# Optimization experiments

Measured on AMD Instinct MI355X. Metric: run time of the kernel, lower is better.

Reference implementation:

```python
import jax, jax.numpy as jnp
import numpy as np

HIDDEN = 1024
HEADS = 16
HEAD_DIM = HIDDEN // HEADS  # 64
MLP_HIDDEN = int(HIDDEN * 4.0)  # 4096
B, L = 2, 2048
EPS_LN = 1e-6
EPS_RMS = 1e-6


def setup_inputs() -> dict:
    key = jax.random.key(0)
    ks = jax.random.split(key, 12)
    s = 0.02
    return {
        "x": jax.random.normal(ks[0], (B, L, HIDDEN), jnp.float32),
        "vec": jax.random.normal(ks[1], (B, HIDDEN), jnp.float32),
        "pe": jax.random.normal(ks[2], (1, 1, L, HEAD_DIM // 2, 2, 2), jnp.float32),
        "w_mod": jax.random.normal(ks[3], (HIDDEN, 3 * HIDDEN), jnp.float32) * s,
        "b_mod": jnp.zeros((3 * HIDDEN,), jnp.float32),
        "w1": jax.random.normal(ks[4], (HIDDEN, 3 * HIDDEN + MLP_HIDDEN), jnp.float32) * s,
        "b1": jnp.zeros((3 * HIDDEN + MLP_HIDDEN,), jnp.float32),
        "w_mlp": jax.random.normal(ks[5], (MLP_HIDDEN, HIDDEN), jnp.float32) * s,
        "b_mlp": jnp.zeros((HIDDEN,), jnp.float32),
        "w2": jax.random.normal(ks[6], (2 * HIDDEN, HIDDEN), jnp.float32) * s,
        "b2": jnp.zeros((HIDDEN,), jnp.float32),
        "q_scale": jnp.ones((HEAD_DIM,), jnp.float32),
        "k_scale": jnp.ones((HEAD_DIM,), jnp.float32),
    }


def _layernorm(x, eps=EPS_LN):
    m = jnp.mean(x, axis=-1, keepdims=True)
    v = jnp.mean(jnp.square(x - m), axis=-1, keepdims=True)
    return (x - m) * jax.lax.rsqrt(v + eps)


def _rmsnorm(x, scale, eps=EPS_RMS):
    rrms = jax.lax.rsqrt(jnp.mean(jnp.square(x), axis=-1, keepdims=True) + eps)
    return x * rrms * scale


def _apply_rope(t, pe):
    # t: [B,H,L,D]; pe: [1,1,L,D//2,2,2]
    t_ = t.reshape(*t.shape[:-1], -1, 1, 2)  # [B,H,L,D//2,1,2]
    out = pe[..., 0] * t_[..., 0] + pe[..., 1] * t_[..., 1]  # [B,H,L,D//2,2]
    return out.reshape(t.shape)


def reference(x, vec, pe, w_mod, b_mod, w1, b1, w_mlp, b_mlp, w2, b2, q_scale, k_scale):
    # adaLN modulation: silu(vec) -> Dense(3*dim) -> shift, scale, gate
    mod = (jax.nn.silu(vec) @ w_mod + b_mod)[:, None, :]  # [B,1,3H]
    shift, scale, gate = jnp.split(mod, 3, axis=-1)
    x_mod = (1.0 + scale) * _layernorm(x) + shift
    # fused QKV + MLP projection
    h = x_mod @ w1 + b1  # [B,L,3H+MH]
    qkv, mlp = h[..., : 3 * HIDDEN], h[..., 3 * HIDDEN :]
    qkv = qkv.reshape(x.shape[0], x.shape[1], 3, HEADS, HEAD_DIM)
    qkv = jnp.transpose(qkv, (2, 0, 3, 1, 4))  # [3,B,H,L,D]
    q, k, v = qkv[0], qkv[1], qkv[2]
    # QK-RMSNorm per head-dim
    q = _rmsnorm(q, q_scale)
    k = _rmsnorm(k, k_scale)
    # RoPE
    q = _apply_rope(q, pe)
    k = _apply_rope(k, pe)
    # attention
    scores = jnp.einsum("bhqd,bhkd->bhqk", q, k) * (HEAD_DIM ** -0.5)
    probs = jax.nn.softmax(scores, axis=-1)
    attn = jnp.einsum("bhqk,bhkd->bhqd", probs, v)
    attn = jnp.transpose(attn, (0, 2, 1, 3)).reshape(x.shape[0], x.shape[1], HIDDEN)
    # mlp branch (Dense with tanh activation per source) + fused output proj
    mlp_out = jnp.tanh(mlp @ w_mlp + b_mlp)
    out = jnp.concatenate([attn, mlp_out], axis=-1) @ w2 + b2
    return x + gate * out
```

## Files before the change

### kernel.cpp

```cpp
#include <hip/hip_runtime.h>
#include <stdint.h>


#define HID  1024
#define NH   16
#define HD   64
#define MLP  4096
#define D1   7168
#define DQKV 3072
#define DCAT 2048
#define BB   2
#define LL   2048
#define TOK  4096

typedef __attribute__((ext_vector_type(8))) short    bf16x8;
typedef __attribute__((ext_vector_type(4))) float    f32x4;
typedef __attribute__((ext_vector_type(4))) unsigned int u32x4;

__device__ __forceinline__ float b2f(unsigned short u) {
    unsigned int v = ((unsigned int)u) << 16;
    float f; __builtin_memcpy(&f, &v, 4); return f;
}
__device__ __forceinline__ unsigned short f2b(float f) {
    unsigned int v; __builtin_memcpy(&v, &f, 4);
    unsigned int r = (v + 0x7FFFu + ((v >> 16) & 1u)) >> 16;
    return (unsigned short)r;
}
__device__ __forceinline__ unsigned int pkbf2(float a, float b) {
    unsigned int ua, ub;
    __builtin_memcpy(&ua, &a, 4); __builtin_memcpy(&ub, &b, 4);
    return ((ua + 0x8000u) >> 16) | ((ub + 0x8000u) & 0xFFFF0000u);
}
__device__ __forceinline__ void gl_lds16(const unsigned short* g, unsigned short* l) {
    __builtin_amdgcn_global_load_lds(
        (const __attribute__((address_space(1))) unsigned int*)(g),
        (__attribute__((address_space(3))) unsigned int*)(l), 16, 0, 0);
}

__global__ void k_transpose_cvt(const float* __restrict__ in,
                                unsigned short* __restrict__ out, int R, int C) {
    __shared__ float tile[32][33];
    int bx = blockIdx.x, by = blockIdx.y;
    int tx = threadIdx.x, ty = threadIdx.y;
    #pragma unroll
    for (int i = 0; i < 4; i++) {
        int r = by * 32 + ty + i * 8;
        int c = bx * 32 + tx;
        tile[ty + i * 8][tx] = in[(size_t)r * C + c];
    }
    __syncthreads();
    #pragma unroll
    for (int i = 0; i < 4; i++) {
        int ro = bx * 32 + ty + i * 8;
        int co = by * 32 + tx;
        out[(size_t)ro * R + co] = f2b(tile[tx][ty + i * 8]);
    }
}

__global__ void k_mod(const float* __restrict__ vec,
                      const float* __restrict__ w_mod,
                      const float* __restrict__ b_mod,
                      float* __restrict__ mod) {
    __shared__ float sv[HID];
    __shared__ float red[8][32];
    int b = blockIdx.y, t = threadIdx.x;
    for (int j = t; j < HID; j += 256) {
        float v = vec[b * HID + j];
        sv[j] = v / (1.0f + __expf(-v));
    }
    __syncthreads();
    int n0 = blockIdx.x * 32;
    int on = t & 31, ks = t >> 5;
    float acc = 0.f;
    const float* wp = w_mod + (size_t)(ks * 128) * 3072 + n0 + on;
    #pragma unroll 4
    for (int k = 0; k < 128; k++) acc += sv[ks * 128 + k] * wp[(size_t)k * 3072];
    red[ks][on] = acc;
    __syncthreads();
    if (t < 32) {
        float s = 0.f;
        #pragma unroll
        for (int i = 0; i < 8; i++) s += red[i][t];
        mod[b * 3072 + n0 + t] = s + b_mod[n0 + t];
    }
}

__global__ void k_lnmod(const float* __restrict__ x,
                        const float* __restrict__ mod,
                        unsigned short* __restrict__ xmod) {
    int tok = blockIdx.x;
    int t = threadIdx.x;
    int b = tok >> 11;
    float4 v4 = *(const float4*)(x + (size_t)tok * HID + t * 4);
    float v0 = v4.x, v1 = v4.y, v2 = v4.z, v3 = v4.w;
    float s  = v0 + v1 + v2 + v3;
    float sq = v0*v0 + v1*v1 + v2*v2 + v3*v3;
    for (int off = 1; off < 64; off <<= 1) {
        s  += __shfl_xor(s,  off);
        sq += __shfl_xor(sq, off);
    }
    __shared__ float ls[4], lq[4];
    int w = t >> 6;
    if ((t & 63) == 0) { ls[w] = s; lq[w] = sq; }
    __syncthreads();
    s  = ls[0] + ls[1] + ls[2] + ls[3];
    sq = lq[0] + lq[1] + lq[2] + lq[3];
    float mean = s * (1.0f / HID);
    float var  = sq * (1.0f / HID) - mean * mean;
    float rstd = rsqrtf(var + 1e-6f);
    const float* mb = mod + b * 3072;
    float y[4] = {v0, v1, v2, v3};
    unsigned short r[4];
    #pragma unroll
    for (int j = 0; j < 4; j++) {
        int col = t * 4 + j;
        float nval = (y[j] - mean) * rstd;
        r[j] = f2b((1.0f + mb[1024 + col]) * nval + mb[col]);
    }
    unsigned int o0 = (unsigned int)r[0] | ((unsigned int)r[1] << 16);
    unsigned int o1 = (unsigned int)r[2] | ((unsigned int)r[3] << 16);
    *(uint2*)(xmod + (size_t)tok * HID + t * 4) = make_uint2(o0, o1);
}

template<int EPI>
__global__ __launch_bounds__(256) void k_gemm(
    const unsigned short* __restrict__ A, int lda,
    const unsigned short* __restrict__ Bt, int ldb,
    const float* __restrict__ bias,
    unsigned short* __restrict__ C, float* __restrict__ Cf, int ldc,
    int K,
    const float* __restrict__ xin,
    const float* __restrict__ mod) {
    __shared__ alignas(16) unsigned short As[128 * 64];
    __shared__ alignas(16) unsigned short Bs[128 * 64];
    int t = threadIdx.x;
    int bm = blockIdx.x, bn = blockIdx.y;
    int lane = t & 63, wave = t >> 6;
    int wm = (wave >> 1) * 64, wn = (wave & 1) * 64;
    int ln = lane & 15, kq = lane >> 4;
    int ln7 = ln & 7;

    f32x4 acc[4][4];
    #pragma unroll
    for (int i = 0; i < 4; i++)
        #pragma unroll
        for (int j = 0; j < 4; j++) acc[i][j] = {0.f, 0.f, 0.f, 0.f};

    int sr  = t >> 3;
    int scg = (t & 7) ^ (sr & 7);
    const unsigned short* Ab = A  + (size_t)(bm * 128) * lda;
    const unsigned short* Bb = Bt + (size_t)(bn * 128) * ldb;

    int ksplit = K / gridDim.z;
    int kbeg = blockIdx.z * ksplit, kend = kbeg + ksplit;

    for (int k0 = kbeg; k0 < kend; k0 += 64) {
        __syncthreads();
        #pragma unroll
        for (int c = 0; c < 4; c++) {
            gl_lds16(Ab + (size_t)(c * 32 + sr) * lda + k0 + scg * 8, &As[c * 2048 + t * 8]);
            gl_lds16(Bb + (size_t)(c * 32 + sr) * ldb + k0 + scg * 8, &Bs[c * 2048 + t * 8]);
        }
        __syncthreads();
        #pragma unroll
        for (int ks = 0; ks < 2; ks++) {
            int slot = ((ks * 4 + kq) ^ ln7) * 8;
            bf16x8 af[4], bfr[4];
            #pragma unroll
            for (int i = 0; i < 4; i++)
                af[i] = *(const bf16x8*)(&As[(wm + i * 16 + ln) * 64 + slot]);
            #pragma unroll
            for (int j = 0; j < 4; j++)
                bfr[j] = *(const bf16x8*)(&Bs[(wn + j * 16 + ln) * 64 + slot]);
            #pragma unroll
            for (int i = 0; i < 4; i++)
                #pragma unroll
                for (int j = 0; j < 4; j++)
                    acc[i][j] = __builtin_amdgcn_mfma_f32_16x16x32_bf16(af[i], bfr[j], acc[i][j], 0, 0, 0);
        }
    }

    #pragma unroll
    for (int i = 0; i < 4; i++) {
        #pragma unroll
        for (int j = 0; j < 4; j++) {
            int col = bn * 128 + wn + j * 16 + ln;
            float bv = (EPI == 3) ? 0.f : bias[col];
            #pragma unroll
            for (int r = 0; r < 4; r++) {
                int row = bm * 128 + wm + i * 16 + kq * 4 + r;
                float v = acc[i][j][r] + bv;
                if (EPI == 0) {
                    C[(size_t)row * ldc + col] = f2b(v);
                } else if (EPI == 1) {
                    C[(size_t)row * ldc + col] = f2b(tanhf(v));
                } else if (EPI == 2) {
                    int b = row >> 11;
                    Cf[(size_t)row * ldc + col] =
                        xin[(size_t)row * HID + col] + mod[b * 3072 + 2048 + col] * v;
                } else {
                    Cf[((size_t)blockIdx.z * TOK + row) * ldc + col] = v;
                }
            }
        }
    }
}

__global__ __launch_bounds__(256) void k_red1(const float* __restrict__ part,
                                              const float* __restrict__ bias,
                                              unsigned short* __restrict__ cat) {
    int idx = blockIdx.x * 256 + threadIdx.x;
    int row = idx >> 8;
    int c4  = (idx & 255) * 4;
    float4 p0 = *(const float4*)(part + (size_t)row * HID + c4);
    float4 p1 = *(const float4*)(part + ((size_t)TOK + row) * HID + c4);
    float4 bv = *(const float4*)(bias + c4);
    float a0 = tanhf(p0.x + p1.x + bv.x);
    float a1 = tanhf(p0.y + p1.y + bv.y);
    float a2 = tanhf(p0.z + p1.z + bv.z);
    float a3 = tanhf(p0.w + p1.w + bv.w);
    *(uint2*)(&cat[(size_t)row * DCAT + HID + c4]) =
        make_uint2(pkbf2(a0, a1), pkbf2(a2, a3));
}

__global__ __launch_bounds__(256) void k_red2(const float* __restrict__ part,
                                              const float* __restrict__ bias,
                                              const float* __restrict__ x,
                                              const float* __restrict__ mod,
                                              float* __restrict__ out) {
    int idx = blockIdx.x * 256 + threadIdx.x;
    int row = idx >> 8;
    int c4  = (idx & 255) * 4;
    int b = row >> 11;
    float4 p0 = *(const float4*)(part + (size_t)row * HID + c4);
    float4 p1 = *(const float4*)(part + ((size_t)TOK + row) * HID + c4);
    float4 bv = *(const float4*)(bias + c4);
    float4 gv = *(const float4*)(mod + b * 3072 + 2048 + c4);
    float4 xv = *(const float4*)(x + (size_t)row * HID + c4);
    float4 o;
    o.x = xv.x + gv.x * (p0.x + p1.x + bv.x);
    o.y = xv.y + gv.y * (p0.y + p1.y + bv.y);
    o.z = xv.z + gv.z * (p0.z + p1.z + bv.z);
    o.w = xv.w + gv.w * (p0.w + p1.w + bv.w);
    *(float4*)(out + (size_t)row * HID + c4) = o;
}

__global__ void k_qkrope(unsigned short* __restrict__ h,
                         const float* __restrict__ pe,
                         const float* __restrict__ q_scale,
                         const float* __restrict__ k_scale) {
    int tok = blockIdx.x;
    int l = tok & (LL - 1);
    int t = threadIdx.x;
    int lane = t & 63, wave = t >> 6;
    int hh = wave * 4 + (lane >> 4);
    int d0 = (lane & 15) * 4;
    unsigned short* row = h + (size_t)tok * D1;
    int i0 = d0 >> 1;
    const float* peb = pe + ((size_t)l * 32 + i0) * 4;
    float4 e0 = *(const float4*)(peb);
    float4 e1 = *(const float4*)(peb + 4);
    #pragma unroll
    for (int qk = 0; qk < 2; qk++) {
        unsigned short* p = row + qk * HID + hh * HD + d0;
        const float* sc = (qk == 0 ? q_scale : k_scale) + d0;
        uint2 qv = *(const uint2*)p;
        float v0 = b2f((unsigned short)(qv.x & 0xFFFF)), v1 = b2f((unsigned short)(qv.x >> 16));
        float v2 = b2f((unsigned short)(qv.y & 0xFFFF)), v3 = b2f((unsigned short)(qv.y >> 16));
        float ssq = v0*v0 + v1*v1 + v2*v2 + v3*v3;
        ssq += __shfl_xor(ssq, 1, 16);
        ssq += __shfl_xor(ssq, 2, 16);
        ssq += __shfl_xor(ssq, 4, 16);
        ssq += __shfl_xor(ssq, 8, 16);
        float rr = rsqrtf(ssq * (1.0f / HD) + 1e-6f);
        if (qk == 0) rr *= 0.18033688011112042f;
        v0 *= rr * sc[0];
        v1 *= rr * sc[1];
        v2 *= rr * sc[2];
        v3 *= rr * sc[3];
        float o0 = e0.x*v0 + e0.y*v1;
        float o1 = e0.z*v0 + e0.w*v1;
        float o2 = e1.x*v2 + e1.y*v3;
        float o3 = e1.z*v2 + e1.w*v3;
        *(uint2*)p = make_uint2(pkbf2(o0, o1), pkbf2(o2, o3));
    }
}

#define KT 64
__global__ __launch_bounds__(256) void k_attn(const unsigned short* __restrict__ h,
                                              unsigned short* __restrict__ cat) {
    __shared__ unsigned short Ks[KT * 64];
    __shared__ unsigned short Vt[HD * 64];
    __shared__ unsigned short Ps[4 * 16 * 64];
    int t = threadIdx.x;
    int bx = blockIdx.x;
    int bh = blockIdx.y;
    int b = bh >> 4, hh = bh & 15;
    int lane = t & 63, w = t >> 6;
    int ln = lane & 15, quad = lane >> 4;
    int ln7 = ln & 7;
    const unsigned short* hb = h + (size_t)b * LL * D1;

    int swk[2];
    swk[0] = ((0 + quad) ^ ln7) * 8;
    swk[1] = ((4 + quad) ^ ln7) * 8;

    bf16x8 qf[2];
    {
        const unsigned short* qbase = hb + (size_t)(bx * 64 + w * 16) * D1 + hh * HD;
        #pragma unroll
        for (int ks = 0; ks < 2; ks++)
            qf[ks] = *(const bf16x8*)(qbase + (size_t)ln * D1 + ks * 32 + quad * 8);
    }

    f32x4 O[4];
    #pragma unroll
    for (int vn = 0; vn < 4; vn++) O[vn] = {0.f, 0.f, 0.f, 0.f};
    float m_ = -1e30f, l_ = 0.f;

    unsigned short* Psw = Ps + w * 16 * 64;

    int skey = t >> 2, sc2 = (t & 3) * 2;
    int p2 = (t & 31) * 2, db = (t >> 5) * 8;

    for (int kb = 0; kb < LL / KT; kb++) {
        __syncthreads();
        {
            const unsigned short* kbase = hb + (size_t)(kb * KT) * D1 + HID + hh * HD;
            u32x4 ka = *(const u32x4*)(kbase + (size_t)skey * D1 + (t & 3) * 16);
            u32x4 kc = *(const u32x4*)(kbase + (size_t)skey * D1 + (t & 3) * 16 + 8);
            int k7 = skey & 7;
            *(u32x4*)(&Ks[skey * 64 + ((sc2 ^ k7) * 8)]) = ka;
            *(u32x4*)(&Ks[skey * 64 + (((sc2 + 1) ^ k7) * 8)]) = kc;
            const unsigned short* vbase = hb + (size_t)(kb * KT) * D1 + 2 * HID + hh * HD;
            u32x4 va = *(const u32x4*)(vbase + (size_t)p2 * D1 + db);
            u32x4 vb = *(const u32x4*)(vbase + (size_t)(p2 + 1) * D1 + db);
            #pragma unroll
            for (int j = 0; j < 8; j++) {
                unsigned int lo = (j & 1) ? (va[j >> 1] >> 16) : (va[j >> 1] & 0xFFFFu);
                unsigned int hi = (j & 1) ? (vb[j >> 1] >> 16) : (vb[j >> 1] & 0xFFFFu);
                int row = db + j;
                *(unsigned int*)(&Vt[row * 64 + (p2 ^ ((row & 7) << 3))]) = lo | (hi << 16);
            }
        }
        __syncthreads();

        f32x4 st[4];
        __builtin_amdgcn_s_setprio(1);
        #pragma unroll
        for (int kt = 0; kt < 4; kt++) {
            st[kt] = {0.f, 0.f, 0.f, 0.f};
            #pragma unroll
            for (int ks = 0; ks < 2; ks++) {
                bf16x8 kf = *(const bf16x8*)(&Ks[(kt * 16 + ln) * 64 + swk[ks]]);
                st[kt] = __builtin_amdgcn_mfma_f32_16x16x32_bf16(kf, qf[ks], st[kt], 0, 0, 0);
            }
        }
        __builtin_amdgcn_s_setprio(0);

        {
            float p[16];
            float mx = -1e30f;
            #pragma unroll
            for (int kt = 0; kt < 4; kt++)
                #pragma unroll
                for (int r = 0; r < 4; r++) {
                    float v = st[kt][r];
                    p[kt * 4 + r] = v;
                    mx = fmaxf(mx, v);
                }
            mx = fmaxf(mx, __shfl_xor(mx, 16));
            mx = fmaxf(mx, __shfl_xor(mx, 32));
            float mnew = fmaxf(m_, mx);
            float alpha = __builtin_amdgcn_exp2f(m_ - mnew);
            m_ = mnew;
            float sum = 0.f;
            #pragma unroll
            for (int i = 0; i < 16; i++) {
                float e = __builtin_amdgcn_exp2f(p[i] - mnew);
                p[i] = e;
                sum += e;
            }
            sum += __shfl_xor(sum, 16);
            sum += __shfl_xor(sum, 32);
            l_ = l_ * alpha + sum;
            #pragma unroll
            for (int vn = 0; vn < 4; vn++)
                #pragma unroll
                for (int r = 0; r < 4; r++) O[vn][r] *= alpha;
            #pragma unroll
            for (int kt = 0; kt < 4; kt++) {
                unsigned long long pk =
                    (unsigned long long)pkbf2(p[kt*4+0], p[kt*4+1])
                  | ((unsigned long long)pkbf2(p[kt*4+2], p[kt*4+3]) << 32);
                int pchunk = (2 * kt + (quad >> 1)) ^ ln7;
                *(unsigned long long*)(&Psw[ln * 64 + pchunk * 8 + (quad & 1) * 4]) = pk;
            }
        }

        __builtin_amdgcn_s_setprio(1);
        #pragma unroll
        for (int kt2 = 0; kt2 < 2; kt2++) {
            bf16x8 pb = *(const bf16x8*)(&Psw[ln * 64 + swk[kt2]]);
            #pragma unroll
            for (int vn = 0; vn < 4; vn++) {
                bf16x8 vf = *(const bf16x8*)(&Vt[(vn * 16 + ln) * 64 + swk[kt2]]);
                O[vn] = __builtin_amdgcn_mfma_f32_16x16x32_bf16(vf, pb, O[vn], 0, 0, 0);
            }
        }
        __builtin_amdgcn_s_setprio(0);
    }

    {
        float rl = 1.0f / l_;
        size_t row = (size_t)(b * LL + bx * 64 + w * 16 + ln);
        #pragma unroll
        for (int vn = 0; vn < 4; vn++) {
            #pragma unroll
            for (int r2 = 0; r2 < 4; r2 += 2) {
                unsigned int pk = pkbf2(O[vn][r2] * rl, O[vn][r2 + 1] * rl);
                *(unsigned int*)(&cat[row * DCAT + hh * HD + vn * 16 + quad * 4 + r2]) = pk;
            }
        }
    }
}

extern "C" void kernel_launch(void* const* d_in, const int* in_sizes, int n_in,
                              void* d_out, int out_size, void* d_ws, size_t ws_size,
                              hipStream_t stream) {
    const float* x       = (const float*)d_in[0];
    const float* vec     = (const float*)d_in[1];
    const float* pe      = (const float*)d_in[2];
    const float* w_mod   = (const float*)d_in[3];
    const float* b_mod   = (const float*)d_in[4];
    const float* w1      = (const float*)d_in[5];
    const float* b1      = (const float*)d_in[6];
    const float* w_mlp   = (const float*)d_in[7];
    const float* b_mlp   = (const float*)d_in[8];
    const float* w2      = (const float*)d_in[9];
    const float* b2      = (const float*)d_in[10];
    const float* q_scale = (const float*)d_in[11];
    const float* k_scale = (const float*)d_in[12];
    float* out = (float*)d_out;

    char* ws = (char*)d_ws;
    size_t off = 0;
    float* mod = (float*)(ws + off);                     off += 6144 * 4;
    unsigned short* xmod  = (unsigned short*)(ws + off); off += (size_t)TOK * HID * 2;
    unsigned short* h     = (unsigned short*)(ws + off); off += (size_t)TOK * D1 * 2;
    unsigned short* cat   = (unsigned short*)(ws + off); off += (size_t)TOK * DCAT * 2;
    unsigned short* w1T   = (unsigned short*)(ws + off); off += (size_t)D1 * HID * 2;
    unsigned short* wmlpT = (unsigned short*)(ws + off); off += (size_t)HID * MLP * 2;
    unsigned short* w2T   = (unsigned short*)(ws + off); off += (size_t)HID * DCAT * 2;
    float* part = (float*)(ws + off);                    off += (size_t)2 * TOK * HID * 4;

    k_transpose_cvt<<<dim3(D1 / 32, HID / 32), dim3(32, 8), 0, stream>>>(w1, w1T, HID, D1);
    k_transpose_cvt<<<dim3(HID / 32, MLP / 32), dim3(32, 8), 0, stream>>>(w_mlp, wmlpT, MLP, HID);
    k_transpose_cvt<<<dim3(HID / 32, DCAT / 32), dim3(32, 8), 0, stream>>>(w2, w2T, DCAT, HID);

    k_mod<<<dim3(96, BB), 256, 0, stream>>>(vec, w_mod, b_mod, mod);
    k_lnmod<<<TOK, 256, 0, stream>>>(x, mod, xmod);

    k_gemm<0><<<dim3(TOK / 128, D1 / 128), 256, 0, stream>>>(
        xmod, HID, w1T, HID, b1, h, nullptr, D1, HID, nullptr, nullptr);

    k_qkrope<<<TOK, 256, 0, stream>>>(h, pe, q_scale, k_scale);

    k_attn<<<dim3(LL / 64, BB * NH), 256, 0, stream>>>(h, cat);

    k_gemm<3><<<dim3(TOK / 128, HID / 128, 2), 256, 0, stream>>>(
        h + DQKV, D1, wmlpT, MLP, b_mlp, nullptr, part, HID, MLP, nullptr, nullptr);
    k_red1<<<TOK * HID / 1024, 256, 0, stream>>>(part, b_mlp, cat);

    k_gemm<3><<<dim3(TOK / 128, HID / 128, 2), 256, 0, stream>>>(
        cat, DCAT, w2T, DCAT, b2, nullptr, part, HID, DCAT, nullptr, nullptr);
    k_red2<<<TOK * HID / 1024, 256, 0, stream>>>(part, b2, x, mod, out);
}
```

Baseline: 409.9 us.

## Add 128x64 split-K GEMM for N=1024 projections and lazy softmax rescale in attention

Introduces a k_gemm64 kernel with 128x64 output tiles and uses it for the MLP-down and output-projection split-K GEMMs, doubling the number of blocks so more CUs are occupied on the narrow N=1024 outputs. In attention, the online-softmax rescale of O and l now runs only when some lane's new max exceeds the running max by more than a threshold, which skips most exp/multiply work per tile. It also switches bf16 packing to the hardware v_cvt_pk_bf16_f32 instruction and uses tree-shaped max and sum reductions. The smaller GEMM tiles lower data reuse per block, and the lazy rescale depends on the threshold staying within fp32 range.

```diff
diff --git a/kernel.cpp b/kernel.cpp
--- a/kernel.cpp
+++ b/kernel.cpp
@@ -30,6 +30,11 @@
     unsigned int ua, ub;
     __builtin_memcpy(&ua, &a, 4); __builtin_memcpy(&ub, &b, 4);
     return ((ua + 0x8000u) >> 16) | ((ub + 0x8000u) & 0xFFFF0000u);
+}
+__device__ __forceinline__ unsigned int cvtpk(float a, float b) {
+    unsigned int r;
+    asm("v_cvt_pk_bf16_f32 %0, %1, %2" : "=v"(r) : "v"(a), "v"(b));
+    return r;
 }
 __device__ __forceinline__ void gl_lds16(const unsigned short* g, unsigned short* l) {
     __builtin_amdgcn_global_load_lds(
@@ -202,6 +207,74 @@
                     Cf[((size_t)blockIdx.z * TOK + row) * ldc + col] = v;
                 }
             }
+        }
+    }
+}
+
+__global__ __launch_bounds__(256) void k_gemm64(
+    const unsigned short* __restrict__ A, int lda,
+    const unsigned short* __restrict__ Bt, int ldb,
+    float* __restrict__ Cf, int ldc,
+    int K) {
+    __shared__ alignas(16) unsigned short As[128 * 64];
+    __shared__ alignas(16) unsigned short Bs[64 * 64];
+    int t = threadIdx.x;
+    int bm = blockIdx.x, bn = blockIdx.y;
+    int lane = t & 63, wave = t >> 6;
+    int wm = wave * 32;
+    int ln = lane & 15, kq = lane >> 4;
+    int ln7 = ln & 7;
+
+    f32x4 acc[2][4];
+    #pragma unroll
+    for (int i = 0; i < 2; i++)
+        #pragma unroll
+        for (int j = 0; j < 4; j++) acc[i][j] = {0.f, 0.f, 0.f, 0.f};
+
+    int sr  = t >> 3;
+    int scg = (t & 7) ^ (sr & 7);
+    const unsigned short* Ab = A  + (size_t)(bm * 128) * lda;
+    const unsigned short* Bb = Bt + (size_t)(bn * 64) * ldb;
+
+    int ksplit = K / gridDim.z;
+    int kbeg = blockIdx.z * ksplit, kend = kbeg + ksplit;
+
+    for (int k0 = kbeg; k0 < kend; k0 += 64) {
+        __syncthreads();
+        #pragma unroll
+        for (int c = 0; c < 4; c++)
+            gl_lds16(Ab + (size_t)(c * 32 + sr) * lda + k0 + scg * 8, &As[c * 2048 + t * 8]);
+        #pragma unroll
+        for (int c = 0; c < 2; c++)
+            gl_lds16(Bb + (size_t)(c * 32 + sr) * ldb + k0 + scg * 8, &Bs[c * 2048 + t * 8]);
+        __syncthreads();
+        #pragma unroll
+        for (int ks = 0; ks < 2; ks++) {
+            int slot = ((ks * 4 + kq) ^ ln7) * 8;
+            bf16x8 af[2], bfr[4];
+            #pragma unroll
+            for (int i = 0; i < 2; i++)
+                af[i] = *(const bf16x8*)(&As[(wm + i * 16 + ln) * 64 + slot]);
+            #pragma unroll
+            for (int j = 0; j < 4; j++)
+                bfr[j] = *(const bf16x8*)(&Bs[(j * 16 + ln) * 64 + slot]);
+            #pragma unroll
+            for (int i = 0; i < 2; i++)
+                #pragma unroll
+                for (int j = 0; j < 4; j++)
+                    acc[i][j] = __builtin_amdgcn_mfma_f32_16x16x32_bf16(af[i], bfr[j], acc[i][j], 0, 0, 0);
+        }
+    }
+
+    #pragma unroll
+    for (int j = 0; j < 4; j++) {
+        int col = bn * 64 + j * 16 + ln;
+        #pragma unroll
+        for (int i = 0; i < 2; i++) {
+            int row = bm * 128 + wm + i * 16 + kq * 4;
+            #pragma unroll
+            for (int r = 0; r < 4; r++)
+                Cf[((size_t)blockIdx.z * TOK + row + r) * ldc + col] = acc[i][j][r];
         }
     }
 }
@@ -360,41 +433,44 @@
 
         {
             float p[16];
-            float mx = -1e30f;
             #pragma unroll
             for (int kt = 0; kt < 4; kt++)
                 #pragma unroll
-                for (int r = 0; r < 4; r++) {
-                    float v = st[kt][r];
-                    p[kt * 4 + r] = v;
-                    mx = fmaxf(mx, v);
-                }
+                for (int r = 0; r < 4; r++) p[kt * 4 + r] = st[kt][r];
+            float a0 = fmaxf(fmaxf(p[0],  p[1]),  p[2]);
+            float a1 = fmaxf(fmaxf(p[3],  p[4]),  p[5]);
+            float a2 = fmaxf(fmaxf(p[6],  p[7]),  p[8]);
+            float a3 = fmaxf(fmaxf(p[9],  p[10]), p[11]);
+            float a4 = fmaxf(fmaxf(p[12], p[13]), p[14]);
+            float mx = fmaxf(fmaxf(fmaxf(a0, a1), a2), fmaxf(fmaxf(a3, a4), p[15]));
             mx = fmaxf(mx, __shfl_xor(mx, 16));
             mx = fmaxf(mx, __shfl_xor(mx, 32));
-            float mnew = fmaxf(m_, mx);
-            float alpha = __builtin_amdgcn_exp2f(m_ - mnew);
-            m_ = mnew;
-            float sum = 0.f;
-            #pragma unroll
-            for (int i = 0; i < 16; i++) {
-                float e = __builtin_amdgcn_exp2f(p[i] - mnew);
-                p[i] = e;
-                sum += e;
-            }
+            if (!__all(mx - m_ <= 10.f)) {
+                float mnew = fmaxf(m_, mx);
+                float alpha = __builtin_amdgcn_exp2f(m_ - mnew);
+                m_ = mnew;
+                l_ *= alpha;
+                #pragma unroll
+                for (int vn = 0; vn < 4; vn++)
+                    #pragma unroll
+                    for (int r = 0; r < 4; r++) O[vn][r] *= alpha;
+            }
+            #pragma unroll
+            for (int i = 0; i < 16; i++) p[i] = __builtin_amdgcn_exp2f(p[i] - m_);
+            float s0 = (p[0] + p[1]) + (p[2] + p[3]);
+            float s1 = (p[4] + p[5]) + (p[6] + p[7]);
+            float s2 = (p[8] + p[9]) + (p[10] + p[11]);
+            float s3 = (p[12] + p[13]) + (p[14] + p[15]);
+            float sum = (s0 + s1) + (s2 + s3);
             sum += __shfl_xor(sum, 16);
             sum += __shfl_xor(sum, 32);
-            l_ = l_ * alpha + sum;
-            #pragma unroll
-            for (int vn = 0; vn < 4; vn++)
-                #pragma unroll
-                for (int r = 0; r < 4; r++) O[vn][r] *= alpha;
+            l_ += sum;
             #pragma unroll
             for (int kt = 0; kt < 4; kt++) {
-                unsigned long long pk =
-                    (unsigned long long)pkbf2(p[kt*4+0], p[kt*4+1])
-                  | ((unsigned long long)pkbf2(p[kt*4+2], p[kt*4+3]) << 32);
+                unsigned int w0 = cvtpk(p[kt*4+0], p[kt*4+1]);
+                unsigned int w1 = cvtpk(p[kt*4+2], p[kt*4+3]);
                 int pchunk = (2 * kt + (quad >> 1)) ^ ln7;
-                *(unsigned long long*)(&Psw[ln * 64 + pchunk * 8 + (quad & 1) * 4]) = pk;
+                *(uint2*)(&Psw[ln * 64 + pchunk * 8 + (quad & 1) * 4]) = make_uint2(w0, w1);
             }
         }
 
@@ -418,7 +494,7 @@
         for (int vn = 0; vn < 4; vn++) {
             #pragma unroll
             for (int r2 = 0; r2 < 4; r2 += 2) {
-                unsigned int pk = pkbf2(O[vn][r2] * rl, O[vn][r2 + 1] * rl);
+                unsigned int pk = cvtpk(O[vn][r2] * rl, O[vn][r2 + 1] * rl);
                 *(unsigned int*)(&cat[row * DCAT + hh * HD + vn * 16 + quad * 4 + r2]) = pk;
             }
         }
@@ -468,11 +544,11 @@
 
     k_attn<<<dim3(LL / 64, BB * NH), 256, 0, stream>>>(h, cat);
 
-    k_gemm<3><<<dim3(TOK / 128, HID / 128, 2), 256, 0, stream>>>(
-        h + DQKV, D1, wmlpT, MLP, b_mlp, nullptr, part, HID, MLP, nullptr, nullptr);
+    k_gemm64<<<dim3(TOK / 128, HID / 64, 2), 256, 0, stream>>>(
+        h + DQKV, D1, wmlpT, MLP, part, HID, MLP);
     k_red1<<<TOK * HID / 1024, 256, 0, stream>>>(part, b_mlp, cat);
 
-    k_gemm<3><<<dim3(TOK / 128, HID / 128, 2), 256, 0, stream>>>(
-        cat, DCAT, w2T, DCAT, b2, nullptr, part, HID, DCAT, nullptr, nullptr);
+    k_gemm64<<<dim3(TOK / 128, HID / 64, 2), 256, 0, stream>>>(
+        cat, DCAT, w2T, DCAT, part, HID, DCAT);
     k_red2<<<TOK * HID / 1024, 256, 0, stream>>>(part, b2, x, mod, out);
 }
```

After: 413.6 us. About the same (+0.9%).

## Pre-transpose V, prefetch K/V tiles, lazy softmax rescale, merge weight transposes

Applied to the files above, without the earlier changes.

Adds a separate kernel that writes V transposed per head, so the attention loop can copy V into LDS with plain vector stores instead of a scalar transpose. K and V loads for the next tile are now issued into registers before the current tile's compute, overlapping global memory latency with MFMA work. The online softmax skips rescaling O and l unless the running max grows by more than a threshold, and conversions to bf16 use the hardware v_cvt_pk_bf16_f32 instruction. The three weight-transpose launches are merged into one; the cost is an extra kernel launch and a V round trip through global memory.

```diff
diff --git a/kernel.cpp b/kernel.cpp
--- a/kernel.cpp
+++ b/kernel.cpp
@@ -31,16 +31,30 @@
     __builtin_memcpy(&ua, &a, 4); __builtin_memcpy(&ub, &b, 4);
     return ((ua + 0x8000u) >> 16) | ((ub + 0x8000u) & 0xFFFF0000u);
 }
+__device__ __forceinline__ unsigned int cvtpk(float a, float b) {
+    unsigned int r;
+    asm("v_cvt_pk_bf16_f32 %0, %1, %2" : "=v"(r) : "v"(a), "v"(b));
+    return r;
+}
 __device__ __forceinline__ void gl_lds16(const unsigned short* g, unsigned short* l) {
     __builtin_amdgcn_global_load_lds(
         (const __attribute__((address_space(1))) unsigned int*)(g),
         (__attribute__((address_space(3))) unsigned int*)(l), 16, 0, 0);
 }
 
-__global__ void k_transpose_cvt(const float* __restrict__ in,
-                                unsigned short* __restrict__ out, int R, int C) {
+__global__ void k_transpose3(const float* __restrict__ w1, unsigned short* __restrict__ w1T,
+                             const float* __restrict__ wmlp, unsigned short* __restrict__ wmlpT,
+                             const float* __restrict__ w2, unsigned short* __restrict__ w2T) {
     __shared__ float tile[32][33];
-    int bx = blockIdx.x, by = blockIdx.y;
+    int id = blockIdx.x;
+    const float* in; unsigned short* out; int R, C, bx, by;
+    if (id < 7168) {
+        in = w1; out = w1T; R = 1024; C = 7168; bx = id % 224; by = id / 224;
+    } else if (id < 11264) {
+        int j = id - 7168; in = wmlp; out = wmlpT; R = 4096; C = 1024; bx = j & 31; by = j >> 5;
+    } else {
+        int j = id - 11264; in = w2; out = w2T; R = 2048; C = 1024; bx = j & 31; by = j >> 5;
+    }
     int tx = threadIdx.x, ty = threadIdx.y;
     #pragma unroll
     for (int i = 0; i < 4; i++) {
@@ -55,6 +69,33 @@
         int co = by * 32 + tx;
         out[(size_t)ro * R + co] = f2b(tile[tx][ty + i * 8]);
     }
+}
+
+__global__ void k_vtrans(const unsigned short* __restrict__ h,
+                         unsigned short* __restrict__ vT) {
+    __shared__ unsigned short tile[64][72];
+    int bh = blockIdx.y;
+    int b = bh >> 4, hh = bh & 15;
+    int l0 = blockIdx.x * 64;
+    int t = threadIdx.x;
+    int r = t >> 2, c8 = (t & 3) * 16;
+    const unsigned short* src = h + (size_t)b * LL * D1 + (size_t)(l0 + r) * D1
+                                  + 2 * HID + hh * HD;
+    u32x4 v0 = *(const u32x4*)(src + c8);
+    u32x4 v1 = *(const u32x4*)(src + c8 + 8);
+    *(u32x4*)(&tile[r][c8]) = v0;
+    *(u32x4*)(&tile[r][c8 + 8]) = v1;
+    __syncthreads();
+    int od = t >> 2, k0 = (t & 3) * 16;
+    unsigned short* dst = vT + ((size_t)bh * 64 + od) * LL + l0 + k0;
+    u32x4 o0, o1;
+    #pragma unroll
+    for (int j = 0; j < 4; j++) {
+        o0[j] = (unsigned int)tile[k0 + 2*j][od] | ((unsigned int)tile[k0 + 2*j + 1][od] << 16);
+        o1[j] = (unsigned int)tile[k0 + 8 + 2*j][od] | ((unsigned int)tile[k0 + 9 + 2*j][od] << 16);
+    }
+    *(u32x4*)(dst) = o0;
+    *(u32x4*)(dst + 8) = o1;
 }
 
 __global__ void k_mod(const float* __restrict__ vec,
@@ -288,6 +329,7 @@
 
 #define KT 64
 __global__ __launch_bounds__(256) void k_attn(const unsigned short* __restrict__ h,
+                                              const unsigned short* __restrict__ vT,
                                               unsigned short* __restrict__ cat) {
     __shared__ unsigned short Ks[KT * 64];
     __shared__ unsigned short Vt[HD * 64];
@@ -320,30 +362,33 @@
 
     unsigned short* Psw = Ps + w * 16 * 64;
 
-    int skey = t >> 2, sc2 = (t & 3) * 2;
-    int p2 = (t & 31) * 2, db = (t >> 5) * 8;
+    int skey = t >> 2, sdc16 = (t & 3) * 16, sc2 = (t & 3) * 2;
+    const unsigned short* kbase0 = hb + HID + hh * HD;
+    const unsigned short* vbase0 = vT + ((size_t)bh * 64 + skey) * LL;
+
+    u32x4 ka = *(const u32x4*)(kbase0 + (size_t)skey * D1 + sdc16);
+    u32x4 kc = *(const u32x4*)(kbase0 + (size_t)skey * D1 + sdc16 + 8);
+    u32x4 va = *(const u32x4*)(vbase0 + sdc16);
+    u32x4 vb = *(const u32x4*)(vbase0 + sdc16 + 8);
 
     for (int kb = 0; kb < LL / KT; kb++) {
         __syncthreads();
         {
-            const unsigned short* kbase = hb + (size_t)(kb * KT) * D1 + HID + hh * HD;
-            u32x4 ka = *(const u32x4*)(kbase + (size_t)skey * D1 + (t & 3) * 16);
-            u32x4 kc = *(const u32x4*)(kbase + (size_t)skey * D1 + (t & 3) * 16 + 8);
             int k7 = skey & 7;
             *(u32x4*)(&Ks[skey * 64 + ((sc2 ^ k7) * 8)]) = ka;
             *(u32x4*)(&Ks[skey * 64 + (((sc2 + 1) ^ k7) * 8)]) = kc;
-            const unsigned short* vbase = hb + (size_t)(kb * KT) * D1 + 2 * HID + hh * HD;
-            u32x4 va = *(const u32x4*)(vbase + (size_t)p2 * D1 + db);
-            u32x4 vb = *(const u32x4*)(vbase + (size_t)(p2 + 1) * D1 + db);
-            #pragma unroll
-            for (int j = 0; j < 8; j++) {
-                unsigned int lo = (j & 1) ? (va[j >> 1] >> 16) : (va[j >> 1] & 0xFFFFu);
-                unsigned int hi = (j & 1) ? (vb[j >> 1] >> 16) : (vb[j >> 1] & 0xFFFFu);
-                int row = db + j;
-                *(unsigned int*)(&Vt[row * 64 + (p2 ^ ((row & 7) << 3))]) = lo | (hi << 16);
-            }
+            *(u32x4*)(&Vt[skey * 64 + ((sc2 ^ k7) * 8)]) = va;
+            *(u32x4*)(&Vt[skey * 64 + (((sc2 + 1) ^ k7) * 8)]) = vb;
         }
         __syncthreads();
+        if (kb + 1 < LL / KT) {
+            const unsigned short* kb1 = kbase0 + (size_t)(kb + 1) * KT * D1;
+            const unsigned short* vb1 = vbase0 + (size_t)(kb + 1) * KT;
+            ka = *(const u32x4*)(kb1 + (size_t)skey * D1 + sdc16);
+            kc = *(const u32x4*)(kb1 + (size_t)skey * D1 + sdc16 + 8);
+            va = *(const u32x4*)(vb1 + sdc16);
+            vb = *(const u32x4*)(vb1 + sdc16 + 8);
+        }
 
         f32x4 st[4];
         __builtin_amdgcn_s_setprio(1);
@@ -360,41 +405,44 @@
 
         {
             float p[16];
-            float mx = -1e30f;
             #pragma unroll
             for (int kt = 0; kt < 4; kt++)
                 #pragma unroll
-                for (int r = 0; r < 4; r++) {
-                    float v = st[kt][r];
-                    p[kt * 4 + r] = v;
-                    mx = fmaxf(mx, v);
-                }
+                for (int r = 0; r < 4; r++) p[kt * 4 + r] = st[kt][r];
+            float a0 = fmaxf(fmaxf(p[0],  p[1]),  p[2]);
+            float a1 = fmaxf(fmaxf(p[3],  p[4]),  p[5]);
+            float a2 = fmaxf(fmaxf(p[6],  p[7]),  p[8]);
+            float a3 = fmaxf(fmaxf(p[9],  p[10]), p[11]);
+            float a4 = fmaxf(fmaxf(p[12], p[13]), p[14]);
+            float mx = fmaxf(fmaxf(fmaxf(a0, a1), a2), fmaxf(fmaxf(a3, a4), p[15]));
             mx = fmaxf(mx, __shfl_xor(mx, 16));
             mx = fmaxf(mx, __shfl_xor(mx, 32));
-            float mnew = fmaxf(m_, mx);
-            float alpha = __builtin_amdgcn_exp2f(m_ - mnew);
-            m_ = mnew;
-            float sum = 0.f;
-            #pragma unroll
-            for (int i = 0; i < 16; i++) {
-                float e = __builtin_amdgcn_exp2f(p[i] - mnew);
-                p[i] = e;
-                sum += e;
+            if (!__all(mx - m_ <= 10.f)) {
+                float mnew = fmaxf(m_, mx);
+                float alpha = __builtin_amdgcn_exp2f(m_ - mnew);
+                m_ = mnew;
+                l_ *= alpha;
+                #pragma unroll
+                for (int vn = 0; vn < 4; vn++)
+                    #pragma unroll
+                    for (int r = 0; r < 4; r++) O[vn][r] *= alpha;
             }
+            #pragma unroll
+            for (int i = 0; i < 16; i++) p[i] = __builtin_amdgcn_exp2f(p[i] - m_);
+            float s0 = (p[0] + p[1]) + (p[2] + p[3]);
+            float s1 = (p[4] + p[5]) + (p[6] + p[7]);
+            float s2 = (p[8] + p[9]) + (p[10] + p[11]);
+            float s3 = (p[12] + p[13]) + (p[14] + p[15]);
+            float sum = (s0 + s1) + (s2 + s3);
             sum += __shfl_xor(sum, 16);
             sum += __shfl_xor(sum, 32);
-            l_ = l_ * alpha + sum;
-            #pragma unroll
-            for (int vn = 0; vn < 4; vn++)
-                #pragma unroll
-                for (int r = 0; r < 4; r++) O[vn][r] *= alpha;
+            l_ += sum;
             #pragma unroll
             for (int kt = 0; kt < 4; kt++) {
-                unsigned long long pk =
-                    (unsigned long long)pkbf2(p[kt*4+0], p[kt*4+1])
-                  | ((unsigned long long)pkbf2(p[kt*4+2], p[kt*4+3]) << 32);
+                unsigned int w0 = cvtpk(p[kt*4+0], p[kt*4+1]);
+                unsigned int w1 = cvtpk(p[kt*4+2], p[kt*4+3]);
                 int pchunk = (2 * kt + (quad >> 1)) ^ ln7;
-                *(unsigned long long*)(&Psw[ln * 64 + pchunk * 8 + (quad & 1) * 4]) = pk;
+                *(uint2*)(&Psw[ln * 64 + pchunk * 8 + (quad & 1) * 4]) = make_uint2(w0, w1);
             }
         }
 
@@ -418,7 +466,7 @@
         for (int vn = 0; vn < 4; vn++) {
             #pragma unroll
             for (int r2 = 0; r2 < 4; r2 += 2) {
-                unsigned int pk = pkbf2(O[vn][r2] * rl, O[vn][r2 + 1] * rl);
+                unsigned int pk = cvtpk(O[vn][r2] * rl, O[vn][r2 + 1] * rl);
                 *(unsigned int*)(&cat[row * DCAT + hh * HD + vn * 16 + quad * 4 + r2]) = pk;
             }
         }
@@ -453,10 +501,9 @@
     unsigned short* wmlpT = (unsigned short*)(ws + off); off += (size_t)HID * MLP * 2;
     unsigned short* w2T   = (unsigned short*)(ws + off); off += (size_t)HID * DCAT * 2;
     float* part = (float*)(ws + off);                    off += (size_t)2 * TOK * HID * 4;
-
-    k_transpose_cvt<<<dim3(D1 / 32, HID / 32), dim3(32, 8), 0, stream>>>(w1, w1T, HID, D1);
-    k_transpose_cvt<<<dim3(HID / 32, MLP / 32), dim3(32, 8), 0, stream>>>(w_mlp, wmlpT, MLP, HID);
-    k_transpose_cvt<<<dim3(HID / 32, DCAT / 32), dim3(32, 8), 0, stream>>>(w2, w2T, DCAT, HID);
+    unsigned short* vT    = (unsigned short*)(ws + off); off += (size_t)BB * NH * HD * LL * 2;
+
+    k_transpose3<<<dim3(13312), dim3(32, 8), 0, stream>>>(w1, w1T, w_mlp, wmlpT, w2, w2T);
 
     k_mod<<<dim3(96, BB), 256, 0, stream>>>(vec, w_mod, b_mod, mod);
     k_lnmod<<<TOK, 256, 0, stream>>>(x, mod, xmod);
@@ -465,8 +512,9 @@
         xmod, HID, w1T, HID, b1, h, nullptr, D1, HID, nullptr, nullptr);
 
     k_qkrope<<<TOK, 256, 0, stream>>>(h, pe, q_scale, k_scale);
-
-    k_attn<<<dim3(LL / 64, BB * NH), 256, 0, stream>>>(h, cat);
+    k_vtrans<<<dim3(LL / 64, BB * NH), 256, 0, stream>>>(h, vT);
+
+    k_attn<<<dim3(LL / 64, BB * NH), 256, 0, stream>>>(h, vT, cat);
 
     k_gemm<3><<<dim3(TOK / 128, HID / 128, 2), 256, 0, stream>>>(
         h + DQKV, D1, wmlpT, MLP, b_mlp, nullptr, part, HID, MLP, nullptr, nullptr);
```

After: 405.7 us. About the same (-1.0%).
